# Performance work log

Measured on AMD Instinct MI355X. Metric: run time of the kernel, lower is better.

Reference implementation:

```python
import jax, jax.numpy as jnp
import numpy as np

B, S, H, D = 8, 1024, 32, 128
SM_SCALE = D ** -0.5


def _make_bias(dtype=jnp.float32):
    # causal mask [1, 1, S, S]
    causal = jnp.tril(jnp.ones((S, S), dtype=bool))[None, None, :, :]
    attn_mask = jnp.ones((B, S), dtype=bool).at[:, S // 2:].set(False)
    pad = attn_mask[:, None, None, :]  # [B,1,1,S]
    combined = jnp.logical_and(causal, pad)  # [B,1,S,S]
    neg = jnp.finfo(dtype).min
    return jnp.where(combined, jnp.asarray(0.0, dtype), jnp.asarray(neg, dtype))


def setup_inputs() -> dict:
    key = jax.random.key(0)
    kq, kk, kv = jax.random.split(key, 3)
    query = jax.random.normal(kq, (B, S, H, D), dtype=jnp.float32)
    k = jax.random.normal(kk, (B, S, H, D), dtype=jnp.float32)
    v = jax.random.normal(kv, (B, S, H, D), dtype=jnp.float32)
    bias = _make_bias()
    return {"query": query, "key": k, "value": v, "bias": bias}


def reference(query, key, value, bias):
    # query/key/value: [B, S, H, D]; bias: [B, 1, Sq, Sk] (broadcast over heads)
    scores = jnp.einsum("bqhd,bkhd->bhqk", query, key) * SM_SCALE + bias
    attn = jax.nn.softmax(scores, axis=-1)
    out = jnp.einsum("bhqk,bkhd->bqhd", attn, value)
    return out
```

## Files before the change

kernel.cpp:

```cpp
#include <hip/hip_runtime.h>
#include <stdint.h>

typedef __attribute__((ext_vector_type(8))) short short8;
typedef __attribute__((ext_vector_type(8))) unsigned short us8;
typedef __attribute__((ext_vector_type(4))) float f32x4;
typedef __attribute__((ext_vector_type(4))) unsigned short usvec4;

#define B_ 8
#define S_ 1024
#define H_ 32
#define D_ 128
#define NSTEP (S_ / 32)

static __device__ __forceinline__ unsigned short f2bf(float f) {
  uint32_t u = __builtin_bit_cast(uint32_t, f);
  u += 0x7FFFu + ((u >> 16) & 1u);
  return (unsigned short)(u >> 16);
}

__global__ __launch_bounds__(256)
void kv_pre(const float* __restrict__ Kp, const float* __restrict__ Vp,
            unsigned short* __restrict__ Kw, unsigned short* __restrict__ Vw)
{
  const int flat   = blockIdx.x * 256 + threadIdx.x;
  const int tid2   = flat & 511;
  const int bhstep = flat >> 9;
  const int step   = bhstep & (NSTEP - 1);
  const int bhi    = bhstep >> 5;
  const int h      = bhi & (H_ - 1);
  const int b      = bhi >> 5;

  const size_t strideS = (size_t)H_ * D_;
  const size_t base    = ((size_t)b * S_) * strideS + (size_t)h * D_;
  const size_t dst     = (size_t)bhstep * 4096 + (size_t)tid2 * 8;

  {
    const int f = tid2 >> 7, tile = (tid2 >> 6) & 1, ln = tid2 & 63;
    const int cc = ln & 15, qd = ln >> 4;
    const float* src = Kp + base + (size_t)(step * 32 + tile * 16 + cc) * strideS + f * 32 + qd * 8;
    float4 a = *(const float4*)src;
    float4 c4 = *(const float4*)(src + 4);
    us8 r;
    r[0] = f2bf(a.x);  r[1] = f2bf(a.y);  r[2] = f2bf(a.z);  r[3] = f2bf(a.w);
    r[4] = f2bf(c4.x); r[5] = f2bf(c4.y); r[6] = f2bf(c4.z); r[7] = f2bf(c4.w);
    *(us8*)(Kw + dst) = r;
  }
  {
    const int t = tid2 >> 6, ln = tid2 & 63;
    const int cv = ln & 15, qv = ln >> 4;
    const float* src = Vp + base + (size_t)(step * 32 + qv * 8) * strideS + t * 16 + cv;
    us8 r;
#pragma unroll
    for (int j = 0; j < 8; ++j) r[j] = f2bf(src[(size_t)j * strideS]);
    *(us8*)(Vw + dst) = r;
  }
}

__global__ __launch_bounds__(256)
void mask_pre(const float* __restrict__ BiasP, uint32_t* __restrict__ Mw)
{
  const int idx = blockIdx.x * 256 + threadIdx.x;
  const float NEGT = -1e37f;
  const float* src = BiasP + (size_t)idx * 32;
  uint32_t mbits = 0;
#pragma unroll
  for (int j = 0; j < 8; ++j) {
    float4 v = *(const float4*)(src + j * 4);
    mbits |= (uint32_t)(v.x > NEGT) << (j * 4 + 0);
    mbits |= (uint32_t)(v.y > NEGT) << (j * 4 + 1);
    mbits |= (uint32_t)(v.z > NEGT) << (j * 4 + 2);
    mbits |= (uint32_t)(v.w > NEGT) << (j * 4 + 3);
  }
  Mw[idx] = mbits;
}

__global__ __launch_bounds__(256, 2)
void fa_fwd2(const float* __restrict__ Qp,
             const unsigned short* __restrict__ Kw,
             const unsigned short* __restrict__ Vw,
             const uint32_t* __restrict__ Mw,
             float* __restrict__ Op)
{
  __shared__ __align__(16) unsigned short klds[2][4096];
  __shared__ __align__(16) unsigned short vlds[2][4096];

  const int tid  = threadIdx.x;
  const int lane = tid & 63;
  const int w    = tid >> 6;
  const int quad = lane >> 4;
  const int c    = lane & 15;

  const int qt = blockIdx.x;
  const int h  = blockIdx.y;
  const int b  = blockIdx.z;
  const int qi = qt * 64 + w * 16 + c;

  const size_t strideS = (size_t)H_ * D_;
  const size_t bh  = ((size_t)b * S_) * strideS + (size_t)h * D_;
  const size_t kvb = (size_t)(b * H_ + h) * ((size_t)NSTEP * 4096);

  short8 qf[4];
  {
    const float* qrow = Qp + bh + (size_t)qi * strideS;
#pragma unroll
    for (int f = 0; f < 4; ++f) {
      float4 a  = *(const float4*)(qrow + f * 32 + quad * 8);
      float4 bv = *(const float4*)(qrow + f * 32 + quad * 8 + 4);
      short8 r;
      r[0] = (short)f2bf(a.x);  r[1] = (short)f2bf(a.y);
      r[2] = (short)f2bf(a.z);  r[3] = (short)f2bf(a.w);
      r[4] = (short)f2bf(bv.x); r[5] = (short)f2bf(bv.y);
      r[6] = (short)f2bf(bv.z); r[7] = (short)f2bf(bv.w);
      qf[f] = r;
    }
  }

  const uint32_t* mrow = Mw + ((size_t)b * S_ + qi) * NSTEP;

  float m  = -INFINITY;
  float ll = 0.f;
  f32x4 acc[8];
#pragma unroll
  for (int t = 0; t < 8; ++t) acc[t] = (f32x4){0.f, 0.f, 0.f, 0.f};

  const float SL2E = 0.08838834764831845f * 1.4426950408889634f;
  int cur = 0;

  for (int st = 0; st < NSTEP; ++st) {
    const uint32_t mw_ = mrow[st];
    const int m0 = (mw_ >> (quad * 4)) & 15;
    const int m1 = (mw_ >> (16 + quad * 4)) & 15;
    const int wv = __any(m0 | m1);
    const int bvalid = __syncthreads_or(wv);
    if (!bvalid) continue;

    {
      const unsigned short* kg = Kw + kvb + (size_t)st * 4096 + w * 1024 + lane * 8;
      const unsigned short* vg = Vw + kvb + (size_t)st * 4096 + w * 1024 + lane * 8;
      unsigned short* kl = &klds[cur][w * 1024];
      unsigned short* vl = &vlds[cur][w * 1024];
#pragma unroll
      for (int i = 0; i < 2; ++i) {
        __builtin_amdgcn_global_load_lds(
            (const __attribute__((address_space(1))) void*)(kg + i * 512),
            (__attribute__((address_space(3))) void*)(kl + i * 512), 16, 0, 0);
        __builtin_amdgcn_global_load_lds(
            (const __attribute__((address_space(1))) void*)(vg + i * 512),
            (__attribute__((address_space(3))) void*)(vl + i * 512), 16, 0, 0);
      }
    }
    __syncthreads();

    if (wv) {
      const unsigned short* kb_ = klds[cur];
      const unsigned short* vb_ = vlds[cur];

      f32x4 st0 = (f32x4){0.f, 0.f, 0.f, 0.f};
      f32x4 st1 = (f32x4){0.f, 0.f, 0.f, 0.f};
      __builtin_amdgcn_s_setprio(1);
#pragma unroll
      for (int f = 0; f < 4; ++f) {
        short8 ka  = *(const short8*)(kb_ + f * 1024 + lane * 8);
        short8 kbt = *(const short8*)(kb_ + f * 1024 + 512 + lane * 8);
        st0 = __builtin_amdgcn_mfma_f32_16x16x32_bf16(ka,  qf[f], st0, 0, 0, 0);
        st1 = __builtin_amdgcn_mfma_f32_16x16x32_bf16(kbt, qf[f], st1, 0, 0, 0);
      }
      __builtin_amdgcn_s_setprio(0);

      float x0[4], x1[4];
      float mt = -INFINITY;
#pragma unroll
      for (int r = 0; r < 4; ++r) {
        x0[r] = ((m0 >> r) & 1) ? st0[r] * SL2E : -INFINITY;
        x1[r] = ((m1 >> r) & 1) ? st1[r] * SL2E : -INFINITY;
        mt = fmaxf(mt, fmaxf(x0[r], x1[r]));
      }
      mt = fmaxf(mt, __shfl_xor(mt, 16));
      mt = fmaxf(mt, __shfl_xor(mt, 32));

      if (!__all(mt <= m + 8.f)) {
        const float mn    = fmaxf(m, mt);
        const float alpha = exp2f(m - mn);
        m = mn;
        ll *= alpha;
#pragma unroll
        for (int t = 0; t < 8; ++t) {
          acc[t][0] *= alpha; acc[t][1] *= alpha;
          acc[t][2] *= alpha; acc[t][3] *= alpha;
        }
      }

      float p0[4], p1[4];
      float lt = 0.f;
#pragma unroll
      for (int r = 0; r < 4; ++r) {
        p0[r] = exp2f(x0[r] - m);
        p1[r] = exp2f(x1[r] - m);
        lt += p0[r] + p1[r];
      }
      lt += __shfl_xor(lt, 16);
      lt += __shfl_xor(lt, 32);
      ll += lt;

      int i0, i1, i2, i3;
      asm("v_cvt_pk_bf16_f32 %0, %1, %2" : "=v"(i0) : "v"(p0[0]), "v"(p0[1]));
      asm("v_cvt_pk_bf16_f32 %0, %1, %2" : "=v"(i1) : "v"(p0[2]), "v"(p0[3]));
      asm("v_cvt_pk_bf16_f32 %0, %1, %2" : "=v"(i2) : "v"(p1[0]), "v"(p1[1]));
      asm("v_cvt_pk_bf16_f32 %0, %1, %2" : "=v"(i3) : "v"(p1[2]), "v"(p1[3]));

      const int srcA = ((quad & 1) << 5) + c;
      const int srcB = srcA + 16;
      const int hiT  = quad >> 1;

      int sA, sB, w0, w1, w2, w3;
      sA = __shfl(i0, srcA); sB = __shfl(i2, srcA); w0 = hiT ? sB : sA;
      sA = __shfl(i1, srcA); sB = __shfl(i3, srcA); w1 = hiT ? sB : sA;
      sA = __shfl(i0, srcB); sB = __shfl(i2, srcB); w2 = hiT ? sB : sA;
      sA = __shfl(i1, srcB); sB = __shfl(i3, srcB); w3 = hiT ? sB : sA;

      union { int u[4]; short8 v; } pf;
      pf.u[0] = w0; pf.u[1] = w1; pf.u[2] = w2; pf.u[3] = w3;

      __builtin_amdgcn_s_setprio(1);
#pragma unroll
      for (int t = 0; t < 8; ++t) {
        short8 vf = *(const short8*)(vb_ + t * 512 + lane * 8);
        acc[t] = __builtin_amdgcn_mfma_f32_16x16x32_bf16(vf, pf.v, acc[t], 0, 0, 0);
      }
      __builtin_amdgcn_s_setprio(0);
    }
    cur ^= 1;
  }

  const float rl = 1.0f / ll;
  float* orow = Op + bh + (size_t)qi * strideS;
#pragma unroll
  for (int t = 0; t < 8; ++t) {
    float4 o;
    o.x = acc[t][0] * rl; o.y = acc[t][1] * rl;
    o.z = acc[t][2] * rl; o.w = acc[t][3] * rl;
    *(float4*)(orow + t * 16 + quad * 4) = o;
  }
}

__global__ __launch_bounds__(256, 2)
void fa_fwd(const float* __restrict__ Qp,
            const float* __restrict__ Kp,
            const float* __restrict__ Vp,
            const float* __restrict__ BiasP,
            float* __restrict__ Op)
{
  __shared__ __align__(16) unsigned short klds[32 * 136];
  __shared__ __align__(16) unsigned short vlds[8 * 520];

  const int tid  = threadIdx.x;
  const int lane = tid & 63;
  const int w    = tid >> 6;
  const int quad = lane >> 4;
  const int c    = lane & 15;

  const int qt = blockIdx.x;
  const int h  = blockIdx.y;
  const int b  = blockIdx.z;
  const int qi = qt * 64 + w * 16 + c;

  const size_t strideS = (size_t)H_ * D_;
  const size_t bh = ((size_t)b * S_) * strideS + (size_t)h * D_;

  short8 qf[4];
  {
    const float* qrow = Qp + bh + (size_t)qi * strideS;
#pragma unroll
    for (int f = 0; f < 4; ++f) {
      float4 a  = *(const float4*)(qrow + f * 32 + quad * 8);
      float4 bv = *(const float4*)(qrow + f * 32 + quad * 8 + 4);
      short8 r;
      r[0] = (short)f2bf(a.x);  r[1] = (short)f2bf(a.y);
      r[2] = (short)f2bf(a.z);  r[3] = (short)f2bf(a.w);
      r[4] = (short)f2bf(bv.x); r[5] = (short)f2bf(bv.y);
      r[6] = (short)f2bf(bv.z); r[7] = (short)f2bf(bv.w);
      qf[f] = r;
    }
  }

  const float* brow = BiasP + ((size_t)b * S_ + qi) * S_;
  const float NEGT = -1e37f;

  float m  = -INFINITY;
  float ll = 0.f;
  f32x4 acc[8];
#pragma unroll
  for (int t = 0; t < 8; ++t) acc[t] = (f32x4){0.f, 0.f, 0.f, 0.f};

  const float SL2E = 0.08838834764831845f * 1.4426950408889634f;
  const float L2E  = 1.4426950408889634f;

  for (int ks = 0; ks < S_; ks += 32) {
    float4 b0f = *(const float4*)(brow + ks + quad * 4);
    float4 b1f = *(const float4*)(brow + ks + 16 + quad * 4);
    float b0a[4] = {b0f.x, b0f.y, b0f.z, b0f.w};
    float b1a[4] = {b1f.x, b1f.y, b1f.z, b1f.w};
    int lv = 0;
#pragma unroll
    for (int r = 0; r < 4; ++r) lv |= (b0a[r] > NEGT) | (b1a[r] > NEGT);
    const int wv = __any(lv);
    const int bvalid = __syncthreads_or(wv);
    if (!bvalid) continue;

    {
      const int kk = tid >> 3;
      const int dc = tid & 7;

      const float* krow = Kp + bh + (size_t)(ks + kk) * strideS + dc * 16;
      unsigned short kb16[16];
#pragma unroll
      for (int i = 0; i < 4; ++i) {
        float4 kv = *(const float4*)(krow + i * 4);
        kb16[i*4+0] = f2bf(kv.x); kb16[i*4+1] = f2bf(kv.y);
        kb16[i*4+2] = f2bf(kv.z); kb16[i*4+3] = f2bf(kv.w);
      }
      usvec4* kdst = (usvec4*)(klds + kk * 136 + dc * 16);
#pragma unroll
      for (int i = 0; i < 4; ++i)
        kdst[i] = (usvec4){kb16[i*4+0], kb16[i*4+1], kb16[i*4+2], kb16[i*4+3]};

      const float* vrow = Vp + bh + (size_t)(ks + kk) * strideS + dc * 16;
      const int base = dc * 520 + (kk >> 3) * 128 + (kk & 7);
#pragma unroll
      for (int i = 0; i < 4; ++i) {
        float4 vv = *(const float4*)(vrow + i * 4);
        vlds[base + (i*4+0)*8] = f2bf(vv.x);
        vlds[base + (i*4+1)*8] = f2bf(vv.y);
        vlds[base + (i*4+2)*8] = f2bf(vv.z);
        vlds[base + (i*4+3)*8] = f2bf(vv.w);
      }
    }
    __syncthreads();

    if (wv) {
      f32x4 st0 = (f32x4){0.f, 0.f, 0.f, 0.f};
      f32x4 st1 = (f32x4){0.f, 0.f, 0.f, 0.f};
#pragma unroll
      for (int f = 0; f < 4; ++f) {
        short8 ka = *(const short8*)(klds + c * 136 + f * 32 + quad * 8);
        short8 kb = *(const short8*)(klds + (16 + c) * 136 + f * 32 + quad * 8);
        st0 = __builtin_amdgcn_mfma_f32_16x16x32_bf16(ka, qf[f], st0, 0, 0, 0);
        st1 = __builtin_amdgcn_mfma_f32_16x16x32_bf16(kb, qf[f], st1, 0, 0, 0);
      }

      float x0[4], x1[4];
      float mt = -INFINITY;
#pragma unroll
      for (int r = 0; r < 4; ++r) {
        x0[r] = (b0a[r] > NEGT) ? fmaf(b0a[r], L2E, st0[r] * SL2E) : -INFINITY;
        x1[r] = (b1a[r] > NEGT) ? fmaf(b1a[r], L2E, st1[r] * SL2E) : -INFINITY;
        mt = fmaxf(mt, fmaxf(x0[r], x1[r]));
      }
      mt = fmaxf(mt, __shfl_xor(mt, 16));
      mt = fmaxf(mt, __shfl_xor(mt, 32));
      const float mn    = fmaxf(m, mt);
      const float alpha = exp2f(m - mn);
      m = mn;

      float p0[4], p1[4];
      float lt = 0.f;
#pragma unroll
      for (int r = 0; r < 4; ++r) {
        p0[r] = exp2f(x0[r] - mn);
        p1[r] = exp2f(x1[r] - mn);
        lt += p0[r] + p1[r];
      }
      lt += __shfl_xor(lt, 16);
      lt += __shfl_xor(lt, 32);
      ll = ll * alpha + lt;

#pragma unroll
      for (int t = 0; t < 8; ++t) {
        acc[t][0] *= alpha; acc[t][1] *= alpha;
        acc[t][2] *= alpha; acc[t][3] *= alpha;
      }

      const int i0 = (int)(((uint32_t)f2bf(p0[0])) | ((uint32_t)f2bf(p0[1]) << 16));
      const int i1 = (int)(((uint32_t)f2bf(p0[2])) | ((uint32_t)f2bf(p0[3]) << 16));
      const int i2 = (int)(((uint32_t)f2bf(p1[0])) | ((uint32_t)f2bf(p1[1]) << 16));
      const int i3 = (int)(((uint32_t)f2bf(p1[2])) | ((uint32_t)f2bf(p1[3]) << 16));

      const int srcA = ((quad & 1) << 5) + c;
      const int srcB = srcA + 16;
      const int hiT  = quad >> 1;

      int sA, sB, w0, w1, w2, w3;
      sA = __shfl(i0, srcA); sB = __shfl(i2, srcA); w0 = hiT ? sB : sA;
      sA = __shfl(i1, srcA); sB = __shfl(i3, srcA); w1 = hiT ? sB : sA;
      sA = __shfl(i0, srcB); sB = __shfl(i2, srcB); w2 = hiT ? sB : sA;
      sA = __shfl(i1, srcB); sB = __shfl(i3, srcB); w3 = hiT ? sB : sA;

      union { int u[4]; short8 v; } pf;
      pf.u[0] = w0; pf.u[1] = w1; pf.u[2] = w2; pf.u[3] = w3;

#pragma unroll
      for (int t = 0; t < 8; ++t) {
        short8 vf = *(const short8*)(vlds + t * 520 + lane * 8);
        acc[t] = __builtin_amdgcn_mfma_f32_16x16x32_bf16(vf, pf.v, acc[t], 0, 0, 0);
      }
    }
    __syncthreads();
  }

  const float rl = 1.0f / ll;
  float* orow = Op + bh + (size_t)qi * strideS;
#pragma unroll
  for (int t = 0; t < 8; ++t) {
    float4 o;
    o.x = acc[t][0] * rl; o.y = acc[t][1] * rl;
    o.z = acc[t][2] * rl; o.w = acc[t][3] * rl;
    *(float4*)(orow + t * 16 + quad * 4) = o;
  }
}

extern "C" void kernel_launch(void* const* d_in, const int* in_sizes, int n_in,
                              void* d_out, int out_size, void* d_ws, size_t ws_size,
                              hipStream_t stream) {
  const float* q    = (const float*)d_in[0];
  const float* k    = (const float*)d_in[1];
  const float* v    = (const float*)d_in[2];
  const float* bias = (const float*)d_in[3];
  float* out = (float*)d_out;

  const size_t KW_BYTES = (size_t)B_ * H_ * NSTEP * 4096 * 2;
  const size_t MW_BYTES = (size_t)B_ * S_ * NSTEP * 4;
  const size_t NEED     = 2 * KW_BYTES + MW_BYTES;

  dim3 grid(S_ / 64, H_, B_);
  if (ws_size >= NEED) {
    unsigned short* Kw = (unsigned short*)d_ws;
    unsigned short* Vw = (unsigned short*)((char*)d_ws + KW_BYTES);
    uint32_t*       Mw = (uint32_t*)((char*)d_ws + 2 * KW_BYTES);
    kv_pre<<<(B_ * H_ * NSTEP * 512) / 256, 256, 0, stream>>>(k, v, Kw, Vw);
    mask_pre<<<(B_ * S_ * NSTEP) / 256, 256, 0, stream>>>(bias, Mw);
    fa_fwd2<<<grid, 256, 0, stream>>>(q, Kw, Vw, Mw, out);
  } else {
    fa_fwd<<<grid, 256, 0, stream>>>(q, k, v, bias, out);
  }
}
```

Baseline: 598.4 us.

## Prefetch next valid K/V tile during compute and skip masked steps upfront

Each block first builds a bitmask of KV steps that have any unmasked entry, using one OR-reduction, instead of a `__syncthreads_or` on every step. The main loop then walks only the set bits. While the current tile is being computed, it issues `global_load_lds` for the next valid tile into the other LDS buffer, so load latency can overlap the MFMA work. Each iteration now ends with one waitcnt plus barrier. In exchange, the kernel gains an upfront pass over 32 mask words per thread and more complex synchronisation around buffer reuse.

```diff
diff --git a/kernel.cpp b/kernel.cpp
--- a/kernel.cpp
+++ b/kernel.cpp
@@ -83,6 +83,7 @@
 {
   __shared__ __align__(16) unsigned short klds[2][4096];
   __shared__ __align__(16) unsigned short vlds[2][4096];
+  __shared__ uint32_t vmask_sh;
 
   const int tid  = threadIdx.x;
   const int lane = tid & 63;
@@ -117,6 +118,26 @@
 
   const uint32_t* mrow = Mw + ((size_t)b * S_ + qi) * NSTEP;
 
+  uint32_t myv = 0;
+#pragma unroll
+  for (int i = 0; i < 8; ++i) {
+    uint4 v = *(const uint4*)(mrow + i * 4);
+    myv |= (uint32_t)(v.x != 0) << (i * 4 + 0);
+    myv |= (uint32_t)(v.y != 0) << (i * 4 + 1);
+    myv |= (uint32_t)(v.z != 0) << (i * 4 + 2);
+    myv |= (uint32_t)(v.w != 0) << (i * 4 + 3);
+  }
+  if (tid == 0) vmask_sh = 0;
+  __syncthreads();
+  {
+    uint32_t wor = myv;
+#pragma unroll
+    for (int d = 1; d < 64; d <<= 1) wor |= __shfl_xor(wor, d);
+    if (lane == 0) atomicOr(&vmask_sh, wor);
+  }
+  __syncthreads();
+  const uint32_t bmask = vmask_sh;
+
   float m  = -INFINITY;
   float ll = 0.f;
   f32x4 acc[8];
@@ -124,34 +145,54 @@
   for (int t = 0; t < 8; ++t) acc[t] = (f32x4){0.f, 0.f, 0.f, 0.f};
 
   const float SL2E = 0.08838834764831845f * 1.4426950408889634f;
+
+  auto stage = [&](int bufi, int stp) {
+    const unsigned short* kg = Kw + kvb + (size_t)stp * 4096 + w * 1024 + lane * 8;
+    const unsigned short* vg = Vw + kvb + (size_t)stp * 4096 + w * 1024 + lane * 8;
+    unsigned short* kl = &klds[bufi][w * 1024];
+    unsigned short* vl = &vlds[bufi][w * 1024];
+    __builtin_amdgcn_global_load_lds(
+        (const __attribute__((address_space(1))) void*)kg,
+        (__attribute__((address_space(3))) void*)kl, 16, 0, 0);
+    __builtin_amdgcn_global_load_lds(
+        (const __attribute__((address_space(1))) void*)(kg + 512),
+        (__attribute__((address_space(3))) void*)(kl + 512), 16, 0, 0);
+    __builtin_amdgcn_global_load_lds(
+        (const __attribute__((address_space(1))) void*)vg,
+        (__attribute__((address_space(3))) void*)vl, 16, 0, 0);
+    __builtin_amdgcn_global_load_lds(
+        (const __attribute__((address_space(1))) void*)(vg + 512),
+        (__attribute__((address_space(3))) void*)(vl + 512), 16, 0, 0);
+  };
+
+  int st  = bmask ? (__ffs(bmask) - 1) : -1;
   int cur = 0;
-
-  for (int st = 0; st < NSTEP; ++st) {
-    const uint32_t mw_ = mrow[st];
-    const int m0 = (mw_ >> (quad * 4)) & 15;
-    const int m1 = (mw_ >> (16 + quad * 4)) & 15;
-    const int wv = __any(m0 | m1);
-    const int bvalid = __syncthreads_or(wv);
-    if (!bvalid) continue;
-
-    {
-      const unsigned short* kg = Kw + kvb + (size_t)st * 4096 + w * 1024 + lane * 8;
-      const unsigned short* vg = Vw + kvb + (size_t)st * 4096 + w * 1024 + lane * 8;
-      unsigned short* kl = &klds[cur][w * 1024];
-      unsigned short* vl = &vlds[cur][w * 1024];
-#pragma unroll
-      for (int i = 0; i < 2; ++i) {
-        __builtin_amdgcn_global_load_lds(
-            (const __attribute__((address_space(1))) void*)(kg + i * 512),
-            (__attribute__((address_space(3))) void*)(kl + i * 512), 16, 0, 0);
-        __builtin_amdgcn_global_load_lds(
-            (const __attribute__((address_space(1))) void*)(vg + i * 512),
-            (__attribute__((address_space(3))) void*)(vl + i * 512), 16, 0, 0);
-      }
-    }
-    __syncthreads();
-
-    if (wv) {
+  uint32_t rem = bmask;
+  uint32_t mw_ = 0;
+
+  if (st >= 0) {
+    mw_ = mrow[st];
+    stage(0, st);
+    asm volatile("s_waitcnt vmcnt(0)" ::: "memory");
+    __builtin_amdgcn_s_barrier();
+    asm volatile("" ::: "memory");
+  }
+
+  while (st >= 0) {
+    rem &= rem - 1;
+    const int nst = rem ? (__ffs(rem) - 1) : -1;
+
+    uint32_t mnxt = 0;
+    if (nst >= 0) {
+      mnxt = mrow[nst];
+      stage(cur ^ 1, nst);
+    }
+
+    const int m0 = (int)((mw_ >> (quad * 4)) & 15u);
+    const int m1 = (int)((mw_ >> (16 + quad * 4)) & 15u);
+    const int wvv = __any(m0 | m1);
+
+    if (wvv) {
       const unsigned short* kb_ = klds[cur];
       const unsigned short* vb_ = vlds[cur];
 
@@ -229,7 +270,15 @@
       }
       __builtin_amdgcn_s_setprio(0);
     }
+
+    if (nst >= 0) {
+      asm volatile("s_waitcnt vmcnt(0)" ::: "memory");
+      __builtin_amdgcn_s_barrier();
+      asm volatile("" ::: "memory");
+    }
     cur ^= 1;
+    st = nst;
+    mw_ = mnxt;
   }
 
   const float rl = 1.0f / ll;
```

New measurement: 551.2 us. -7.9%, faster.
